# Performance work log

Measured on AMD Instinct MI355X. Metric: run time of the kernel, lower is better.

The kernel has to match this reference:

```python
import jax, jax.numpy as jnp
import numpy as np

N_NODES = 1_000_000
MEM_DIM = 128
MSG_DIM = 256
N_UPD = 200_000


def setup_inputs() -> dict:
    key = jax.random.key(0)
    k0, k1, k2, k3, k4 = jax.random.split(key, 5)
    memory = jax.random.normal(k0, (N_NODES, MEM_DIM), dtype=jnp.float32)
    last_update = jnp.zeros((N_NODES,), dtype=jnp.float32)
    # 'unique' node ids: arange guarantees uniqueness and in-range values
    unique_node_ids = jnp.arange(N_UPD, dtype=jnp.int32)
    unique_messages = jax.random.normal(k1, (N_UPD, MSG_DIM), dtype=jnp.float32)
    timestamps = jax.random.uniform(k2, (N_UPD,), dtype=jnp.float32) * 1000.0
    # torch.nn.GRUCell parameters (the TGN memory_updater)
    scale = 1.0 / np.sqrt(MEM_DIM)
    W_ih = jax.random.uniform(k3, (3 * MEM_DIM, MSG_DIM), jnp.float32, -scale, scale)
    W_hh = jax.random.uniform(k4, (3 * MEM_DIM, MEM_DIM), jnp.float32, -scale, scale)
    b_ih = jnp.zeros((3 * MEM_DIM,), jnp.float32)
    b_hh = jnp.zeros((3 * MEM_DIM,), jnp.float32)
    return {
        "memory": memory,
        "last_update": last_update,
        "unique_node_ids": unique_node_ids,
        "unique_messages": unique_messages,
        "timestamps": timestamps,
        "W_ih": W_ih,
        "W_hh": W_hh,
        "b_ih": b_ih,
        "b_hh": b_hh,
    }


def _gru_cell(x, h, W_ih, W_hh, b_ih, b_hh):
    # torch.nn.GRUCell math
    gi = x @ W_ih.T + b_ih          # [U, 3H]
    gh = h @ W_hh.T + b_hh          # [U, 3H]
    i_r, i_z, i_n = jnp.split(gi, 3, axis=-1)
    h_r, h_z, h_n = jnp.split(gh, 3, axis=-1)
    r = jax.nn.sigmoid(i_r + h_r)
    z = jax.nn.sigmoid(i_z + h_z)
    n = jnp.tanh(i_n + r * h_n)
    return (1.0 - z) * n + z * h


def reference(memory, last_update, unique_node_ids, unique_messages, timestamps,
              W_ih, W_hh, b_ih, b_hh):
    # gather rows of the node memory (get_memory / updated_memory[unique_node_ids])
    h = memory[unique_node_ids]                              # [U, H]
    new_h = _gru_cell(unique_messages, h, W_ih, W_hh, b_ih, b_hh)
    # scatter updated rows back (set_memory) and update timestamps
    updated_memory = memory.at[unique_node_ids].set(new_h)
    updated_last_update = last_update.at[unique_node_ids].set(timestamps)
    return updated_memory, updated_last_update
```

## Files before the change

kernel.cpp:

```cpp
#include <hip/hip_runtime.h>
#include <hip/hip_bf16.h>
#include <stdint.h>

#define MEM_DIM 128
#define MSG_DIM 256
#define NGATE   384
#define NQ      512
#define KTOT    384
#define BM      64
#define BK      32
#define NKSTEP  (KTOT / BK)

typedef __attribute__((ext_vector_type(8))) __bf16 bf16x8;
typedef __attribute__((ext_vector_type(4))) float  f32x4;

union B8u { uint32_t u[4]; bf16x8 v; };

__device__ __forceinline__ uint32_t cvt_pk(float lo, float hi) {
    uint32_t r;
    asm("v_cvt_pk_bf16_f32 %0, %1, %2" : "=v"(r) : "v"(lo), "v"(hi));
    return r;
}

__device__ __forceinline__ bf16x8 load_cvt8(const float* __restrict__ p) {
    f32x4 a = *(const f32x4*)p;
    f32x4 b = *(const f32x4*)(p + 4);
    B8u r;
    r.u[0] = cvt_pk(a.x, a.y);
    r.u[1] = cvt_pk(a.z, a.w);
    r.u[2] = cvt_pk(b.x, b.y);
    r.u[3] = cvt_pk(b.z, b.w);
    return r.v;
}

__device__ __forceinline__ bf16x8 zero8() {
    B8u r; r.u[0] = r.u[1] = r.u[2] = r.u[3] = 0; return r.v;
}

__device__ __forceinline__ float sigm(float x) {
    return __builtin_amdgcn_rcpf(1.0f + __expf(-x));
}
__device__ __forceinline__ float tanh_fast(float x) {
    return 1.0f - 2.0f * __builtin_amdgcn_rcpf(1.0f + __expf(2.0f * x));
}

__global__ void bm_zero_kernel(uint32_t* __restrict__ bm, int nwords) {
    int i = blockIdx.x * 256 + threadIdx.x;
    if (i < nwords) bm[i] = 0;
}
__global__ void bm_set_kernel(const int* __restrict__ ids, uint32_t* __restrict__ bm, int U) {
    int i = blockIdx.x * 256 + threadIdx.x;
    if (i < U) {
        int id = ids[i];
        atomicOr(&bm[id >> 5], 1u << (id & 31));
    }
}

__global__ void copy_skip_kernel(const f32x4* __restrict__ mem,
                                 const float* __restrict__ lu,
                                 f32x4* __restrict__ outm,
                                 float* __restrict__ outlu,
                                 const uint32_t* __restrict__ bm,
                                 int NN) {
    const int64_t n_mem_chunks = (int64_t)NN * 32;
    const int64_t total = n_mem_chunks + NN;
    const int64_t stride = (int64_t)gridDim.x * blockDim.x;
    for (int64_t i = (int64_t)blockIdx.x * blockDim.x + threadIdx.x; i < total; i += stride) {
        if (i < n_mem_chunks) {
            int row = (int)(i >> 5);
            if (!((bm[row >> 5] >> (row & 31)) & 1u)) {
                f32x4 v = __builtin_nontemporal_load(&mem[i]);
                __builtin_nontemporal_store(v, &outm[i]);
            }
        } else {
            int node = (int)(i - n_mem_chunks);
            if (!((bm[node >> 5] >> (node & 31)) & 1u))
                outlu[node] = lu[node];
        }
    }
}

__global__ void copy_all_kernel(const f32x4* __restrict__ mem,
                                const f32x4* __restrict__ lu,
                                f32x4* __restrict__ out,
                                int n_mem4, int n_tot4) {
    int stride = gridDim.x * blockDim.x;
    for (int i = blockIdx.x * blockDim.x + threadIdx.x; i < n_tot4; i += stride) {
        f32x4 v = (i < n_mem4) ? mem[i]
                               : __builtin_nontemporal_load(&lu[i - n_mem4]);
        __builtin_nontemporal_store(v, &out[i]);
    }
}

__global__ void wcat_kernel(const float* __restrict__ wih,
                            const float* __restrict__ whh,
                            __hip_bfloat16* __restrict__ wcat) {
    int i = blockIdx.x * 256 + threadIdx.x;
    if (i >= NQ * KTOT) return;
    int lr = i / KTOT, k = i - lr * KTOT;
    int q = lr >> 7, c = lr & 127;
    float v;
    if (k < MSG_DIM) {
        int g = (q == 2) ? 2 : q;
        v = (q == 3) ? 0.f : wih[(size_t)(g * MEM_DIM + c) * MSG_DIM + k];
    } else {
        int g = (q == 3) ? 2 : q;
        v = (q == 2) ? 0.f : whh[(size_t)(g * MEM_DIM + c) * MEM_DIM + (k - MSG_DIM)];
    }
    wcat[i] = __float2bfloat16(v);
}

__device__ __forceinline__ int at_addr(int row, int kbyte) {
    return (row * (KTOT * 2) + kbyte) ^ ((row & 7) << 4);
}
__device__ __forceinline__ int bt_addr(int lr, int kbyte) {
    return (lr * (BK * 2) + kbyte) ^ ((lr & 7) << 4);
}

template<bool PRE>
__global__ __launch_bounds__(512, 4)
void gru_gemm_kernel(const float* __restrict__ memory,
                     const int*   __restrict__ ids,
                     const float* __restrict__ msgs,
                     const float* __restrict__ ts,
                     const float* __restrict__ Wih,
                     const float* __restrict__ Whh,
                     const float* __restrict__ bih,
                     const float* __restrict__ bhh,
                     const __hip_bfloat16* __restrict__ Wcat,
                     float* __restrict__ out_mem,
                     float* __restrict__ out_lu,
                     int U) {
    __shared__ __align__(16) char At[BM * KTOT * 2];
    __shared__ __align__(16) char Bt[NQ * BK * 2];

    const int tid  = threadIdx.x;
    const int w    = tid >> 6;
    const int lane = tid & 63;
    const int lq   = lane & 15;
    const int lk   = lane >> 4;
    const int rb   = blockIdx.x * BM;

    if (tid < BM) {
        int r = rb + tid;
        if (r < U) out_lu[ids[r]] = ts[r];
    }

    {
        int r = tid >> 3, seg = tid & 7;
        int rA = rb + r; if (rA >= U) rA = U - 1;
        const float* xp = msgs + (size_t)rA * MSG_DIM + seg * 32;
        #pragma unroll
        for (int i = 0; i < 4; ++i)
            *(bf16x8*)(At + at_addr(r, seg * 64 + i * 16)) = load_cvt8(xp + i * 8);
    }
    if (tid < 256) {
        int r = tid >> 2, seg = tid & 3;
        int rA = rb + r; if (rA >= U) rA = U - 1;
        const float* hp = memory + (size_t)ids[rA] * MEM_DIM + seg * 32;
        #pragma unroll
        for (int i = 0; i < 4; ++i)
            *(bf16x8*)(At + at_addr(r, 512 + seg * 64 + i * 16)) = load_cvt8(hp + i * 8);
    }

    const int c = w * 16 + lq;
    const float br  = bih[c] + bhh[c];
    const float bz  = bih[MEM_DIM + c] + bhh[MEM_DIM + c];
    const float bin = bih[2 * MEM_DIM + c];
    const float bhn = bhh[2 * MEM_DIM + c];

    const f32x4 z4 = {0.f, 0.f, 0.f, 0.f};
    f32x4 acc[4][4];
    #pragma unroll
    for (int m = 0; m < 4; ++m)
        #pragma unroll
        for (int q = 0; q < 4; ++q) acc[m][q] = z4;

    const int br_ = tid ^ ((tid & 1) << 2);
    const int bq  = br_ >> 7, bc = br_ & 127;

    for (int ks = 0; ks < NKSTEP; ++ks) {
        __syncthreads();
        if (PRE) {
            const __hip_bfloat16* wp = Wcat + (size_t)br_ * KTOT + ks * BK;
            #pragma unroll
            for (int i = 0; i < 4; ++i)
                *(bf16x8*)(Bt + bt_addr(br_, i * 16)) = *(const bf16x8*)(wp + i * 8);
        } else {
            bool isx = (ks < 8);
            bool zero = isx ? (bq == 3) : (bq == 2);
            const float* src;
            if (isx) {
                int g = (bq == 2) ? 2 : bq;
                src = Wih + (size_t)(g * MEM_DIM + bc) * MSG_DIM + ks * BK;
            } else {
                int g = (bq == 3) ? 2 : bq;
                src = Whh + (size_t)(g * MEM_DIM + bc) * MEM_DIM + (ks - 8) * BK;
            }
            #pragma unroll
            for (int i = 0; i < 4; ++i)
                *(bf16x8*)(Bt + bt_addr(br_, i * 16)) =
                    zero ? zero8() : load_cvt8(src + i * 8);
        }
        __syncthreads();

        bf16x8 af[4];
        #pragma unroll
        for (int m = 0; m < 4; ++m)
            af[m] = *(const bf16x8*)(At + at_addr(m * 16 + lq, ks * 64 + lk * 16));

        #pragma unroll
        for (int q = 0; q < 4; ++q) {
            bf16x8 bf_ = *(const bf16x8*)(Bt + bt_addr(q * 128 + w * 16 + lq, lk * 16));
            #pragma unroll
            for (int m = 0; m < 4; ++m)
                acc[m][q] = __builtin_amdgcn_mfma_f32_16x16x32_bf16(af[m], bf_, acc[m][q], 0, 0, 0);
        }
    }

    #pragma unroll
    for (int m = 0; m < 4; ++m) {
        #pragma unroll
        for (int j = 0; j < 4; ++j) {
            int row = m * 16 + lk * 4 + j;
            int r = rb + row;
            if (r < U) {
                int id = ids[r];
                float hold = __bfloat162float(
                    *(const __hip_bfloat16*)(At + at_addr(row, 512 + c * 2)));
                float rg = sigm(acc[m][0][j] + br);
                float zg = sigm(acc[m][1][j] + bz);
                float ng = tanh_fast(acc[m][2][j] + bin + rg * (acc[m][3][j] + bhn));
                out_mem[(size_t)id * MEM_DIM + c] = (1.0f - zg) * ng + zg * hold;
            }
        }
    }
}

extern "C" void kernel_launch(void* const* d_in, const int* in_sizes, int n_in,
                              void* d_out, int out_size, void* d_ws, size_t ws_size,
                              hipStream_t stream) {
    const float* memory      = (const float*)d_in[0];
    const float* last_update = (const float*)d_in[1];
    const int*   ids         = (const int*)  d_in[2];
    const float* msgs        = (const float*)d_in[3];
    const float* ts          = (const float*)d_in[4];
    const float* Wih         = (const float*)d_in[5];
    const float* Whh         = (const float*)d_in[6];
    const float* bih         = (const float*)d_in[7];
    const float* bhh         = (const float*)d_in[8];

    const int NN = in_sizes[1];
    const int U  = in_sizes[2];

    float* out_mem = (float*)d_out;
    float* out_lu  = out_mem + (size_t)NN * MEM_DIM;

    const size_t WCAT_BYTES = (size_t)NQ * KTOT * sizeof(__hip_bfloat16);
    const size_t BM_OFF     = (WCAT_BYTES + 255) & ~(size_t)255;
    const int    BMWORDS    = (NN + 31) / 32;
    const int    nblocks    = (U + BM - 1) / BM;

    if (ws_size >= BM_OFF + (size_t)BMWORDS * 4) {
        __hip_bfloat16* wcat = (__hip_bfloat16*)d_ws;
        uint32_t* bm = (uint32_t*)((char*)d_ws + BM_OFF);

        wcat_kernel<<<(NQ * KTOT + 255) / 256, 256, 0, stream>>>(Wih, Whh, wcat);
        bm_zero_kernel<<<(BMWORDS + 255) / 256, 256, 0, stream>>>(bm, BMWORDS);
        bm_set_kernel<<<(U + 255) / 256, 256, 0, stream>>>(ids, bm, U);

        gru_gemm_kernel<true><<<nblocks, 512, 0, stream>>>(memory, ids, msgs, ts,
                                                           Wih, Whh, bih, bhh, wcat,
                                                           out_mem, out_lu, U);

        copy_skip_kernel<<<8192, 256, 0, stream>>>((const f32x4*)memory, last_update,
                                                   (f32x4*)out_mem, out_lu, bm, NN);
    } else {
        int n_mem4 = NN * MEM_DIM / 4;
        int n_tot4 = n_mem4 + NN / 4;
        copy_all_kernel<<<8192, 256, 0, stream>>>((const f32x4*)memory,
                                                  (const f32x4*)last_update,
                                                  (f32x4*)d_out, n_mem4, n_tot4);
        gru_gemm_kernel<false><<<nblocks, 512, 0, stream>>>(memory, ids, msgs, ts,
                                                            Wih, Whh, bih, bhh, nullptr,
                                                            out_mem, out_lu, U);
    }
}
```

Measured before the change: 412.6 us.

## Fuse GRU GEMM with skip-copy in persistent kernel and drop zero-padded gate tiles

```diff
diff --git a/kernel.cpp b/kernel.cpp
--- a/kernel.cpp
+++ b/kernel.cpp
@@ -4,12 +4,10 @@
 
 #define MEM_DIM 128
 #define MSG_DIM 256
-#define NGATE   384
-#define NQ      512
 #define KTOT    384
 #define BM      64
 #define BK      32
-#define NKSTEP  (KTOT / BK)
+#define NBROW   384
 
 typedef __attribute__((ext_vector_type(8))) __bf16 bf16x8;
 typedef __attribute__((ext_vector_type(4))) float  f32x4;
@@ -33,10 +31,6 @@
     return r.v;
 }
 
-__device__ __forceinline__ bf16x8 zero8() {
-    B8u r; r.u[0] = r.u[1] = r.u[2] = r.u[3] = 0; return r.v;
-}
-
 __device__ __forceinline__ float sigm(float x) {
     return __builtin_amdgcn_rcpf(1.0f + __expf(-x));
 }
@@ -56,28 +50,14 @@
     }
 }
 
-__global__ void copy_skip_kernel(const f32x4* __restrict__ mem,
-                                 const float* __restrict__ lu,
-                                 f32x4* __restrict__ outm,
-                                 float* __restrict__ outlu,
-                                 const uint32_t* __restrict__ bm,
-                                 int NN) {
-    const int64_t n_mem_chunks = (int64_t)NN * 32;
-    const int64_t total = n_mem_chunks + NN;
-    const int64_t stride = (int64_t)gridDim.x * blockDim.x;
-    for (int64_t i = (int64_t)blockIdx.x * blockDim.x + threadIdx.x; i < total; i += stride) {
-        if (i < n_mem_chunks) {
-            int row = (int)(i >> 5);
-            if (!((bm[row >> 5] >> (row & 31)) & 1u)) {
-                f32x4 v = __builtin_nontemporal_load(&mem[i]);
-                __builtin_nontemporal_store(v, &outm[i]);
-            }
-        } else {
-            int node = (int)(i - n_mem_chunks);
-            if (!((bm[node >> 5] >> (node & 31)) & 1u))
-                outlu[node] = lu[node];
-        }
-    }
+__global__ void wconv_kernel(const float* __restrict__ wih,
+                             const float* __restrict__ whh,
+                             __hip_bfloat16* __restrict__ out) {
+    int i = blockIdx.x * 256 + threadIdx.x;
+    const int NIH = 3 * MEM_DIM * MSG_DIM;
+    const int NHH = 3 * MEM_DIM * MEM_DIM;
+    if (i < NIH)            out[i] = __float2bfloat16(wih[i]);
+    else if (i < NIH + NHH) out[i] = __float2bfloat16(whh[i - NIH]);
 }
 
 __global__ void copy_all_kernel(const f32x4* __restrict__ mem,
@@ -92,24 +72,6 @@
     }
 }
 
-__global__ void wcat_kernel(const float* __restrict__ wih,
-                            const float* __restrict__ whh,
-                            __hip_bfloat16* __restrict__ wcat) {
-    int i = blockIdx.x * 256 + threadIdx.x;
-    if (i >= NQ * KTOT) return;
-    int lr = i / KTOT, k = i - lr * KTOT;
-    int q = lr >> 7, c = lr & 127;
-    float v;
-    if (k < MSG_DIM) {
-        int g = (q == 2) ? 2 : q;
-        v = (q == 3) ? 0.f : wih[(size_t)(g * MEM_DIM + c) * MSG_DIM + k];
-    } else {
-        int g = (q == 3) ? 2 : q;
-        v = (q == 2) ? 0.f : whh[(size_t)(g * MEM_DIM + c) * MEM_DIM + (k - MSG_DIM)];
-    }
-    wcat[i] = __float2bfloat16(v);
-}
-
 __device__ __forceinline__ int at_addr(int row, int kbyte) {
     return (row * (KTOT * 2) + kbyte) ^ ((row & 7) << 4);
 }
@@ -117,51 +79,31 @@
     return (lr * (BK * 2) + kbyte) ^ ((lr & 7) << 4);
 }
 
-template<bool PRE>
-__global__ __launch_bounds__(512, 4)
-void gru_gemm_kernel(const float* __restrict__ memory,
-                     const int*   __restrict__ ids,
-                     const float* __restrict__ msgs,
-                     const float* __restrict__ ts,
-                     const float* __restrict__ Wih,
-                     const float* __restrict__ Whh,
-                     const float* __restrict__ bih,
-                     const float* __restrict__ bhh,
-                     const __hip_bfloat16* __restrict__ Wcat,
-                     float* __restrict__ out_mem,
-                     float* __restrict__ out_lu,
-                     int U) {
+template<bool PRE, bool COPY>
+__global__ __launch_bounds__(512)
+void gru_fused_kernel(const float* __restrict__ memory,
+                      const int*   __restrict__ ids,
+                      const float* __restrict__ msgs,
+                      const float* __restrict__ ts,
+                      const float* __restrict__ Wih,
+                      const float* __restrict__ Whh,
+                      const float* __restrict__ bih,
+                      const float* __restrict__ bhh,
+                      const __hip_bfloat16* __restrict__ WihB,
+                      const __hip_bfloat16* __restrict__ WhhB,
+                      const uint32_t* __restrict__ bm,
+                      const float* __restrict__ last_update,
+                      float* __restrict__ out_mem,
+                      float* __restrict__ out_lu,
+                      int U, int ntiles, int NN) {
     __shared__ __align__(16) char At[BM * KTOT * 2];
-    __shared__ __align__(16) char Bt[NQ * BK * 2];
+    __shared__ __align__(16) char Bt[NBROW * BK * 2];
 
     const int tid  = threadIdx.x;
     const int w    = tid >> 6;
     const int lane = tid & 63;
     const int lq   = lane & 15;
     const int lk   = lane >> 4;
-    const int rb   = blockIdx.x * BM;
-
-    if (tid < BM) {
-        int r = rb + tid;
-        if (r < U) out_lu[ids[r]] = ts[r];
-    }
-
-    {
-        int r = tid >> 3, seg = tid & 7;
-        int rA = rb + r; if (rA >= U) rA = U - 1;
-        const float* xp = msgs + (size_t)rA * MSG_DIM + seg * 32;
-        #pragma unroll
-        for (int i = 0; i < 4; ++i)
-            *(bf16x8*)(At + at_addr(r, seg * 64 + i * 16)) = load_cvt8(xp + i * 8);
-    }
-    if (tid < 256) {
-        int r = tid >> 2, seg = tid & 3;
-        int rA = rb + r; if (rA >= U) rA = U - 1;
-        const float* hp = memory + (size_t)ids[rA] * MEM_DIM + seg * 32;
-        #pragma unroll
-        for (int i = 0; i < 4; ++i)
-            *(bf16x8*)(At + at_addr(r, 512 + seg * 64 + i * 16)) = load_cvt8(hp + i * 8);
-    }
 
     const int c = w * 16 + lq;
     const float br  = bih[c] + bhh[c];
@@ -170,68 +112,163 @@
     const float bhn = bhh[2 * MEM_DIM + c];
 
     const f32x4 z4 = {0.f, 0.f, 0.f, 0.f};
-    f32x4 acc[4][4];
-    #pragma unroll
-    for (int m = 0; m < 4; ++m)
+
+    #pragma unroll 1
+    for (int t = blockIdx.x; t < ntiles; t += gridDim.x) {
+        const int rb = t * BM;
+
+        bf16x8 pre[3];
         #pragma unroll
-        for (int q = 0; q < 4; ++q) acc[m][q] = z4;
-
-    const int br_ = tid ^ ((tid & 1) << 2);
-    const int bq  = br_ >> 7, bc = br_ & 127;
-
-    for (int ks = 0; ks < NKSTEP; ++ks) {
+        for (int k = 0; k < 3; ++k) {
+            int chunk = tid + k * 512;
+            int row = chunk >> 2, seg = chunk & 3;
+            if (PRE) pre[k] = *(const bf16x8*)(WihB + row * MSG_DIM + seg * 8);
+            else     pre[k] = load_cvt8(Wih + (size_t)row * MSG_DIM + seg * 8);
+        }
+
         __syncthreads();
-        if (PRE) {
-            const __hip_bfloat16* wp = Wcat + (size_t)br_ * KTOT + ks * BK;
+
+        {
+            int r = tid >> 3, seg = tid & 7;
+            int rA = rb + r; if (rA >= U) rA = U - 1;
+            const float* xp = msgs + (size_t)rA * MSG_DIM + seg * 32;
             #pragma unroll
             for (int i = 0; i < 4; ++i)
-                *(bf16x8*)(Bt + bt_addr(br_, i * 16)) = *(const bf16x8*)(wp + i * 8);
-        } else {
-            bool isx = (ks < 8);
-            bool zero = isx ? (bq == 3) : (bq == 2);
-            const float* src;
-            if (isx) {
-                int g = (bq == 2) ? 2 : bq;
-                src = Wih + (size_t)(g * MEM_DIM + bc) * MSG_DIM + ks * BK;
-            } else {
-                int g = (bq == 3) ? 2 : bq;
-                src = Whh + (size_t)(g * MEM_DIM + bc) * MEM_DIM + (ks - 8) * BK;
-            }
-            #pragma unroll
-            for (int i = 0; i < 4; ++i)
-                *(bf16x8*)(Bt + bt_addr(br_, i * 16)) =
-                    zero ? zero8() : load_cvt8(src + i * 8);
-        }
-        __syncthreads();
-
-        bf16x8 af[4];
+                *(bf16x8*)(At + at_addr(r, seg * 64 + i * 16)) = load_cvt8(xp + i * 8);
+        }
+        {
+            int r = tid >> 3, u = tid & 7;
+            int rA = rb + r; if (rA >= U) rA = U - 1;
+            const float* hp = memory + (size_t)ids[rA] * MEM_DIM + u * 16;
+            *(bf16x8*)(At + at_addr(r, 512 + u * 32))      = load_cvt8(hp);
+            *(bf16x8*)(At + at_addr(r, 512 + u * 32 + 16)) = load_cvt8(hp + 8);
+        }
+        if (tid < BM) {
+            int r = rb + tid;
+            if (r < U) out_lu[ids[r]] = ts[r];
+        }
+
+        f32x4 acc[4][4];
         #pragma unroll
         for (int m = 0; m < 4; ++m)
-            af[m] = *(const bf16x8*)(At + at_addr(m * 16 + lq, ks * 64 + lk * 16));
+            #pragma unroll
+            for (int q = 0; q < 4; ++q) acc[m][q] = z4;
+
+        #pragma unroll 1
+        for (int ks = 0; ks < 8; ++ks) {
+            __syncthreads();
+            #pragma unroll
+            for (int k = 0; k < 3; ++k) {
+                int chunk = tid + k * 512;
+                int row = chunk >> 2, seg = chunk & 3;
+                *(bf16x8*)(Bt + bt_addr(row, seg * 16)) = pre[k];
+            }
+            __syncthreads();
+            {
+                const bool nx = (ks + 1 < 8);
+                const int ksl = nx ? (ks + 1) : 0;
+                #pragma unroll
+                for (int k = 0; k < 3; ++k) {
+                    int chunk = tid + k * 512;
+                    int row = chunk >> 2, seg = chunk & 3;
+                    if (PRE) pre[k] = nx ? *(const bf16x8*)(WihB + row * MSG_DIM + ksl * BK + seg * 8)
+                                         : *(const bf16x8*)(WhhB + row * MEM_DIM + seg * 8);
+                    else     pre[k] = nx ? load_cvt8(Wih + (size_t)row * MSG_DIM + ksl * BK + seg * 8)
+                                         : load_cvt8(Whh + (size_t)row * MEM_DIM + seg * 8);
+                }
+            }
+            bf16x8 af[4];
+            #pragma unroll
+            for (int m = 0; m < 4; ++m)
+                af[m] = *(const bf16x8*)(At + at_addr(m * 16 + lq, ks * 64 + lk * 16));
+            #pragma unroll
+            for (int q = 0; q < 3; ++q) {
+                bf16x8 bv = *(const bf16x8*)(Bt + bt_addr(q * 128 + w * 16 + lq, lk * 16));
+                #pragma unroll
+                for (int m = 0; m < 4; ++m)
+                    acc[m][q] = __builtin_amdgcn_mfma_f32_16x16x32_bf16(af[m], bv, acc[m][q], 0, 0, 0);
+            }
+        }
+        #pragma unroll 1
+        for (int ks = 8; ks < 12; ++ks) {
+            __syncthreads();
+            #pragma unroll
+            for (int k = 0; k < 3; ++k) {
+                int chunk = tid + k * 512;
+                int row = chunk >> 2, seg = chunk & 3;
+                *(bf16x8*)(Bt + bt_addr(row, seg * 16)) = pre[k];
+            }
+            __syncthreads();
+            if (ks < 11) {
+                const int ksl = ks + 1 - 8;
+                #pragma unroll
+                for (int k = 0; k < 3; ++k) {
+                    int chunk = tid + k * 512;
+                    int row = chunk >> 2, seg = chunk & 3;
+                    if (PRE) pre[k] = *(const bf16x8*)(WhhB + row * MEM_DIM + ksl * BK + seg * 8);
+                    else     pre[k] = load_cvt8(Whh + (size_t)row * MEM_DIM + ksl * BK + seg * 8);
+                }
+            }
+            bf16x8 af[4];
+            #pragma unroll
+            for (int m = 0; m < 4; ++m)
+                af[m] = *(const bf16x8*)(At + at_addr(m * 16 + lq, ks * 64 + lk * 16));
+            {
+                bf16x8 bv = *(const bf16x8*)(Bt + bt_addr(0 * 128 + w * 16 + lq, lk * 16));
+                #pragma unroll
+                for (int m = 0; m < 4; ++m)
+                    acc[m][0] = __builtin_amdgcn_mfma_f32_16x16x32_bf16(af[m], bv, acc[m][0], 0, 0, 0);
+            }
+            {
+                bf16x8 bv = *(const bf16x8*)(Bt + bt_addr(1 * 128 + w * 16 + lq, lk * 16));
+                #pragma unroll
+                for (int m = 0; m < 4; ++m)
+                    acc[m][1] = __builtin_amdgcn_mfma_f32_16x16x32_bf16(af[m], bv, acc[m][1], 0, 0, 0);
+            }
+            {
+                bf16x8 bv = *(const bf16x8*)(Bt + bt_addr(2 * 128 + w * 16 + lq, lk * 16));
+                #pragma unroll
+                for (int m = 0; m < 4; ++m)
+                    acc[m][3] = __builtin_amdgcn_mfma_f32_16x16x32_bf16(af[m], bv, acc[m][3], 0, 0, 0);
+            }
+        }
 
         #pragma unroll
-        for (int q = 0; q < 4; ++q) {
-            bf16x8 bf_ = *(const bf16x8*)(Bt + bt_addr(q * 128 + w * 16 + lq, lk * 16));
-            #pragma unroll
-            for (int m = 0; m < 4; ++m)
-                acc[m][q] = __builtin_amdgcn_mfma_f32_16x16x32_bf16(af[m], bf_, acc[m][q], 0, 0, 0);
-        }
-    }
-
-    #pragma unroll
-    for (int m = 0; m < 4; ++m) {
-        #pragma unroll
-        for (int j = 0; j < 4; ++j) {
-            int row = m * 16 + lk * 4 + j;
-            int r = rb + row;
-            if (r < U) {
-                int id = ids[r];
-                float hold = __bfloat162float(
-                    *(const __hip_bfloat16*)(At + at_addr(row, 512 + c * 2)));
-                float rg = sigm(acc[m][0][j] + br);
-                float zg = sigm(acc[m][1][j] + bz);
-                float ng = tanh_fast(acc[m][2][j] + bin + rg * (acc[m][3][j] + bhn));
-                out_mem[(size_t)id * MEM_DIM + c] = (1.0f - zg) * ng + zg * hold;
+        for (int m = 0; m < 4; ++m) {
+            #pragma unroll
+            for (int j = 0; j < 4; ++j) {
+                int row = m * 16 + lk * 4 + j;
+                int r = rb + row;
+                if (r < U) {
+                    int id = ids[r];
+                    float hold = __bfloat162float(
+                        *(const __hip_bfloat16*)(At + at_addr(row, 512 + c * 2)));
+                    float rg = sigm(acc[m][0][j] + br);
+                    float zg = sigm(acc[m][1][j] + bz);
+                    float ng = tanh_fast(acc[m][2][j] + bin + rg * (acc[m][3][j] + bhn));
+                    out_mem[(size_t)id * MEM_DIM + c] = (1.0f - zg) * ng + zg * hold;
+                }
+            }
+        }
+    }
+
+    if (COPY) {
+        const int64_t n_mem_chunks = (int64_t)NN * 32;
+        const int64_t total = n_mem_chunks + NN;
+        const int64_t stride = (int64_t)gridDim.x * blockDim.x;
+        const f32x4* memv = (const f32x4*)memory;
+        f32x4* outv = (f32x4*)out_mem;
+        for (int64_t i = (int64_t)blockIdx.x * blockDim.x + tid; i < total; i += stride) {
+            if (i < n_mem_chunks) {
+                int row = (int)(i >> 5);
+                if (!((bm[row >> 5] >> (row & 31)) & 1u)) {
+                    f32x4 v = __builtin_nontemporal_load(&memv[i]);
+                    __builtin_nontemporal_store(v, &outv[i]);
+                }
+            } else {
+                int node = (int)(i - n_mem_chunks);
+                if (!((bm[node >> 5] >> (node & 31)) & 1u))
+                    out_lu[node] = last_update[node];
             }
         }
     }
@@ -256,33 +293,33 @@
     float* out_mem = (float*)d_out;
     float* out_lu  = out_mem + (size_t)NN * MEM_DIM;
 
-    const size_t WCAT_BYTES = (size_t)NQ * KTOT * sizeof(__hip_bfloat16);
-    const size_t BM_OFF     = (WCAT_BYTES + 255) & ~(size_t)255;
-    const int    BMWORDS    = (NN + 31) / 32;
-    const int    nblocks    = (U + BM - 1) / BM;
+    const int NIH = 3 * MEM_DIM * MSG_DIM;
+    const int NHH = 3 * MEM_DIM * MEM_DIM;
+    const size_t WBYTES  = (size_t)(NIH + NHH) * sizeof(__hip_bfloat16);
+    const size_t BM_OFF  = (WBYTES + 255) & ~(size_t)255;
+    const int    BMWORDS = (NN + 31) / 32;
+    const int    ntiles  = (U + BM - 1) / BM;
+    const int    GRID    = 512;
 
     if (ws_size >= BM_OFF + (size_t)BMWORDS * 4) {
-        __hip_bfloat16* wcat = (__hip_bfloat16*)d_ws;
+        __hip_bfloat16* wb = (__hip_bfloat16*)d_ws;
         uint32_t* bm = (uint32_t*)((char*)d_ws + BM_OFF);
 
-        wcat_kernel<<<(NQ * KTOT + 255) / 256, 256, 0, stream>>>(Wih, Whh, wcat);
+        wconv_kernel<<<(NIH + NHH + 255) / 256, 256, 0, stream>>>(Wih, Whh, wb);
         bm_zero_kernel<<<(BMWORDS + 255) / 256, 256, 0, stream>>>(bm, BMWORDS);
         bm_set_kernel<<<(U + 255) / 256, 256, 0, stream>>>(ids, bm, U);
 
-        gru_gemm_kernel<true><<<nblocks, 512, 0, stream>>>(memory, ids, msgs, ts,
-                                                           Wih, Whh, bih, bhh, wcat,
-                                                           out_mem, out_lu, U);
-
-        copy_skip_kernel<<<8192, 256, 0, stream>>>((const f32x4*)memory, last_update,
-                                                   (f32x4*)out_mem, out_lu, bm, NN);
+        gru_fused_kernel<true, true><<<GRID, 512, 0, stream>>>(
+            memory, ids, msgs, ts, Wih, Whh, bih, bhh,
+            wb, wb + NIH, bm, last_update, out_mem, out_lu, U, ntiles, NN);
     } else {
         int n_mem4 = NN * MEM_DIM / 4;
         int n_tot4 = n_mem4 + NN / 4;
         copy_all_kernel<<<8192, 256, 0, stream>>>((const f32x4*)memory,
                                                   (const f32x4*)last_update,
                                                   (f32x4*)d_out, n_mem4, n_tot4);
-        gru_gemm_kernel<false><<<nblocks, 512, 0, stream>>>(memory, ids, msgs, ts,
-                                                            Wih, Whh, bih, bhh, nullptr,
-                                                            out_mem, out_lu, U);
-    }
-}
+        gru_fused_kernel<false, false><<<GRID, 512, 0, stream>>>(
+            memory, ids, msgs, ts, Wih, Whh, bih, bhh,
+            nullptr, nullptr, nullptr, last_update, out_mem, out_lu, U, ntiles, NN);
+    }
+}
```

Result: slower. 500.3 us (+21.3%).

## Stream GRU weights from global into registers and skip zero-padded gate blocks

Applied to the files above, without the earlier changes.

```diff
diff --git a/kernel.cpp b/kernel.cpp
--- a/kernel.cpp
+++ b/kernel.cpp
@@ -4,12 +4,8 @@
 
 #define MEM_DIM 128
 #define MSG_DIM 256
-#define NGATE   384
-#define NQ      512
 #define KTOT    384
 #define BM      64
-#define BK      32
-#define NKSTEP  (KTOT / BK)
 
 typedef __attribute__((ext_vector_type(8))) __bf16 bf16x8;
 typedef __attribute__((ext_vector_type(4))) float  f32x4;
@@ -33,10 +29,6 @@
     return r.v;
 }
 
-__device__ __forceinline__ bf16x8 zero8() {
-    B8u r; r.u[0] = r.u[1] = r.u[2] = r.u[3] = 0; return r.v;
-}
-
 __device__ __forceinline__ float sigm(float x) {
     return __builtin_amdgcn_rcpf(1.0f + __expf(-x));
 }
@@ -54,6 +46,16 @@
         int id = ids[i];
         atomicOr(&bm[id >> 5], 1u << (id & 31));
     }
+}
+
+__global__ void wconv_kernel(const float* __restrict__ wih,
+                             const float* __restrict__ whh,
+                             __hip_bfloat16* __restrict__ out) {
+    int i = blockIdx.x * 256 + threadIdx.x;
+    const int NIH = 3 * MEM_DIM * MSG_DIM;
+    const int NHH = 3 * MEM_DIM * MEM_DIM;
+    if (i < NIH)            out[i] = __float2bfloat16(wih[i]);
+    else if (i < NIH + NHH) out[i] = __float2bfloat16(whh[i - NIH]);
 }
 
 __global__ void copy_skip_kernel(const f32x4* __restrict__ mem,
@@ -92,47 +94,26 @@
     }
 }
 
-__global__ void wcat_kernel(const float* __restrict__ wih,
-                            const float* __restrict__ whh,
-                            __hip_bfloat16* __restrict__ wcat) {
-    int i = blockIdx.x * 256 + threadIdx.x;
-    if (i >= NQ * KTOT) return;
-    int lr = i / KTOT, k = i - lr * KTOT;
-    int q = lr >> 7, c = lr & 127;
-    float v;
-    if (k < MSG_DIM) {
-        int g = (q == 2) ? 2 : q;
-        v = (q == 3) ? 0.f : wih[(size_t)(g * MEM_DIM + c) * MSG_DIM + k];
-    } else {
-        int g = (q == 3) ? 2 : q;
-        v = (q == 2) ? 0.f : whh[(size_t)(g * MEM_DIM + c) * MEM_DIM + (k - MSG_DIM)];
-    }
-    wcat[i] = __float2bfloat16(v);
-}
-
 __device__ __forceinline__ int at_addr(int row, int kbyte) {
     return (row * (KTOT * 2) + kbyte) ^ ((row & 7) << 4);
 }
-__device__ __forceinline__ int bt_addr(int lr, int kbyte) {
-    return (lr * (BK * 2) + kbyte) ^ ((lr & 7) << 4);
-}
 
 template<bool PRE>
 __global__ __launch_bounds__(512, 4)
-void gru_gemm_kernel(const float* __restrict__ memory,
-                     const int*   __restrict__ ids,
-                     const float* __restrict__ msgs,
-                     const float* __restrict__ ts,
-                     const float* __restrict__ Wih,
-                     const float* __restrict__ Whh,
-                     const float* __restrict__ bih,
-                     const float* __restrict__ bhh,
-                     const __hip_bfloat16* __restrict__ Wcat,
-                     float* __restrict__ out_mem,
-                     float* __restrict__ out_lu,
-                     int U) {
+void gru_stream_kernel(const float* __restrict__ memory,
+                       const int*   __restrict__ ids,
+                       const float* __restrict__ msgs,
+                       const float* __restrict__ ts,
+                       const float* __restrict__ Wih,
+                       const float* __restrict__ Whh,
+                       const float* __restrict__ bih,
+                       const float* __restrict__ bhh,
+                       const __hip_bfloat16* __restrict__ WihB,
+                       const __hip_bfloat16* __restrict__ WhhB,
+                       float* __restrict__ out_mem,
+                       float* __restrict__ out_lu,
+                       int U) {
     __shared__ __align__(16) char At[BM * KTOT * 2];
-    __shared__ __align__(16) char Bt[NQ * BK * 2];
 
     const int tid  = threadIdx.x;
     const int w    = tid >> 6;
@@ -154,13 +135,12 @@
         for (int i = 0; i < 4; ++i)
             *(bf16x8*)(At + at_addr(r, seg * 64 + i * 16)) = load_cvt8(xp + i * 8);
     }
-    if (tid < 256) {
-        int r = tid >> 2, seg = tid & 3;
+    {
+        int r = tid >> 3, u = tid & 7;
         int rA = rb + r; if (rA >= U) rA = U - 1;
-        const float* hp = memory + (size_t)ids[rA] * MEM_DIM + seg * 32;
-        #pragma unroll
-        for (int i = 0; i < 4; ++i)
-            *(bf16x8*)(At + at_addr(r, 512 + seg * 64 + i * 16)) = load_cvt8(hp + i * 8);
+        const float* hp = memory + (size_t)ids[rA] * MEM_DIM + u * 16;
+        *(bf16x8*)(At + at_addr(r, 512 + u * 32))      = load_cvt8(hp);
+        *(bf16x8*)(At + at_addr(r, 512 + u * 32 + 16)) = load_cvt8(hp + 8);
     }
 
     const int c = w * 16 + lq;
@@ -169,6 +149,11 @@
     const float bin = bih[2 * MEM_DIM + c];
     const float bhn = bhh[2 * MEM_DIM + c];
 
+    const __hip_bfloat16* wih_l = WihB + c * MSG_DIM + lk * 8;
+    const __hip_bfloat16* whh_l = WhhB + c * MEM_DIM + lk * 8;
+    const float* wih_f = Wih + c * MSG_DIM + lk * 8;
+    const float* whh_f = Whh + c * MEM_DIM + lk * 8;
+
     const f32x4 z4 = {0.f, 0.f, 0.f, 0.f};
     f32x4 acc[4][4];
     #pragma unroll
@@ -176,46 +161,59 @@
         #pragma unroll
         for (int q = 0; q < 4; ++q) acc[m][q] = z4;
 
-    const int br_ = tid ^ ((tid & 1) << 2);
-    const int bq  = br_ >> 7, bc = br_ & 127;
-
-    for (int ks = 0; ks < NKSTEP; ++ks) {
-        __syncthreads();
+    __syncthreads();
+
+    #pragma unroll 1
+    for (int ks = 0; ks < 8; ++ks) {
+        bf16x8 bv0, bv1, bv2;
         if (PRE) {
-            const __hip_bfloat16* wp = Wcat + (size_t)br_ * KTOT + ks * BK;
-            #pragma unroll
-            for (int i = 0; i < 4; ++i)
-                *(bf16x8*)(Bt + bt_addr(br_, i * 16)) = *(const bf16x8*)(wp + i * 8);
+            bv0 = *(const bf16x8*)(wih_l + 0 * 128 * MSG_DIM + ks * 32);
+            bv1 = *(const bf16x8*)(wih_l + 1 * 128 * MSG_DIM + ks * 32);
+            bv2 = *(const bf16x8*)(wih_l + 2 * 128 * MSG_DIM + ks * 32);
         } else {
-            bool isx = (ks < 8);
-            bool zero = isx ? (bq == 3) : (bq == 2);
-            const float* src;
-            if (isx) {
-                int g = (bq == 2) ? 2 : bq;
-                src = Wih + (size_t)(g * MEM_DIM + bc) * MSG_DIM + ks * BK;
-            } else {
-                int g = (bq == 3) ? 2 : bq;
-                src = Whh + (size_t)(g * MEM_DIM + bc) * MEM_DIM + (ks - 8) * BK;
-            }
-            #pragma unroll
-            for (int i = 0; i < 4; ++i)
-                *(bf16x8*)(Bt + bt_addr(br_, i * 16)) =
-                    zero ? zero8() : load_cvt8(src + i * 8);
-        }
-        __syncthreads();
-
+            bv0 = load_cvt8(wih_f + 0 * 128 * MSG_DIM + ks * 32);
+            bv1 = load_cvt8(wih_f + 1 * 128 * MSG_DIM + ks * 32);
+            bv2 = load_cvt8(wih_f + 2 * 128 * MSG_DIM + ks * 32);
+        }
         bf16x8 af[4];
         #pragma unroll
         for (int m = 0; m < 4; ++m)
             af[m] = *(const bf16x8*)(At + at_addr(m * 16 + lq, ks * 64 + lk * 16));
-
-        #pragma unroll
-        for (int q = 0; q < 4; ++q) {
-            bf16x8 bf_ = *(const bf16x8*)(Bt + bt_addr(q * 128 + w * 16 + lq, lk * 16));
-            #pragma unroll
-            for (int m = 0; m < 4; ++m)
-                acc[m][q] = __builtin_amdgcn_mfma_f32_16x16x32_bf16(af[m], bf_, acc[m][q], 0, 0, 0);
-        }
+        #pragma unroll
+        for (int m = 0; m < 4; ++m)
+            acc[m][0] = __builtin_amdgcn_mfma_f32_16x16x32_bf16(af[m], bv0, acc[m][0], 0, 0, 0);
+        #pragma unroll
+        for (int m = 0; m < 4; ++m)
+            acc[m][1] = __builtin_amdgcn_mfma_f32_16x16x32_bf16(af[m], bv1, acc[m][1], 0, 0, 0);
+        #pragma unroll
+        for (int m = 0; m < 4; ++m)
+            acc[m][2] = __builtin_amdgcn_mfma_f32_16x16x32_bf16(af[m], bv2, acc[m][2], 0, 0, 0);
+    }
+    #pragma unroll 1
+    for (int ks = 0; ks < 4; ++ks) {
+        bf16x8 bv0, bv1, bv2;
+        if (PRE) {
+            bv0 = *(const bf16x8*)(whh_l + 0 * 128 * MEM_DIM + ks * 32);
+            bv1 = *(const bf16x8*)(whh_l + 1 * 128 * MEM_DIM + ks * 32);
+            bv2 = *(const bf16x8*)(whh_l + 2 * 128 * MEM_DIM + ks * 32);
+        } else {
+            bv0 = load_cvt8(whh_f + 0 * 128 * MEM_DIM + ks * 32);
+            bv1 = load_cvt8(whh_f + 1 * 128 * MEM_DIM + ks * 32);
+            bv2 = load_cvt8(whh_f + 2 * 128 * MEM_DIM + ks * 32);
+        }
+        bf16x8 af[4];
+        #pragma unroll
+        for (int m = 0; m < 4; ++m)
+            af[m] = *(const bf16x8*)(At + at_addr(m * 16 + lq, 512 + ks * 64 + lk * 16));
+        #pragma unroll
+        for (int m = 0; m < 4; ++m)
+            acc[m][0] = __builtin_amdgcn_mfma_f32_16x16x32_bf16(af[m], bv0, acc[m][0], 0, 0, 0);
+        #pragma unroll
+        for (int m = 0; m < 4; ++m)
+            acc[m][1] = __builtin_amdgcn_mfma_f32_16x16x32_bf16(af[m], bv1, acc[m][1], 0, 0, 0);
+        #pragma unroll
+        for (int m = 0; m < 4; ++m)
+            acc[m][3] = __builtin_amdgcn_mfma_f32_16x16x32_bf16(af[m], bv2, acc[m][3], 0, 0, 0);
     }
 
     #pragma unroll
@@ -256,22 +254,24 @@
     float* out_mem = (float*)d_out;
     float* out_lu  = out_mem + (size_t)NN * MEM_DIM;
 
-    const size_t WCAT_BYTES = (size_t)NQ * KTOT * sizeof(__hip_bfloat16);
-    const size_t BM_OFF     = (WCAT_BYTES + 255) & ~(size_t)255;
-    const int    BMWORDS    = (NN + 31) / 32;
-    const int    nblocks    = (U + BM - 1) / BM;
+    const int NIH = 3 * MEM_DIM * MSG_DIM;
+    const int NHH = 3 * MEM_DIM * MEM_DIM;
+    const size_t WBYTES  = (size_t)(NIH + NHH) * sizeof(__hip_bfloat16);
+    const size_t BM_OFF  = (WBYTES + 255) & ~(size_t)255;
+    const int    BMWORDS = (NN + 31) / 32;
+    const int    nblocks = (U + BM - 1) / BM;
 
     if (ws_size >= BM_OFF + (size_t)BMWORDS * 4) {
-        __hip_bfloat16* wcat = (__hip_bfloat16*)d_ws;
+        __hip_bfloat16* wb = (__hip_bfloat16*)d_ws;
         uint32_t* bm = (uint32_t*)((char*)d_ws + BM_OFF);
 
-        wcat_kernel<<<(NQ * KTOT + 255) / 256, 256, 0, stream>>>(Wih, Whh, wcat);
+        wconv_kernel<<<(NIH + NHH + 255) / 256, 256, 0, stream>>>(Wih, Whh, wb);
         bm_zero_kernel<<<(BMWORDS + 255) / 256, 256, 0, stream>>>(bm, BMWORDS);
         bm_set_kernel<<<(U + 255) / 256, 256, 0, stream>>>(ids, bm, U);
 
-        gru_gemm_kernel<true><<<nblocks, 512, 0, stream>>>(memory, ids, msgs, ts,
-                                                           Wih, Whh, bih, bhh, wcat,
-                                                           out_mem, out_lu, U);
+        gru_stream_kernel<true><<<nblocks, 512, 0, stream>>>(
+            memory, ids, msgs, ts, Wih, Whh, bih, bhh,
+            wb, wb + NIH, out_mem, out_lu, U);
 
         copy_skip_kernel<<<8192, 256, 0, stream>>>((const f32x4*)memory, last_update,
                                                    (f32x4*)out_mem, out_lu, bm, NN);
@@ -281,8 +281,8 @@
         copy_all_kernel<<<8192, 256, 0, stream>>>((const f32x4*)memory,
                                                   (const f32x4*)last_update,
                                                   (f32x4*)d_out, n_mem4, n_tot4);
-        gru_gemm_kernel<false><<<nblocks, 512, 0, stream>>>(memory, ids, msgs, ts,
-                                                            Wih, Whh, bih, bhh, nullptr,
-                                                            out_mem, out_lu, U);
-    }
-}
+        gru_stream_kernel<false><<<nblocks, 512, 0, stream>>>(
+            memory, ids, msgs, ts, Wih, Whh, bih, bhh,
+            nullptr, nullptr, out_mem, out_lu, U);
+    }
+}
```

New measurement: 353.4 us. 14.3% less time.
